# Kernel optimization log

Measured on AMD Instinct MI355X. Metric: run time of the kernel, lower is better.

The kernel has to match this reference:

```python
import jax, jax.numpy as jnp
import numpy as np

B, N, E = 2, 30000, 120000
IN_F, OUT_F, H = 512, 512, 4
D = OUT_F // H  # head_dim = 128
LN_EPS = 1e-5


def setup_inputs() -> dict:
    key = jax.random.key(0)
    k1, k2, k3, k4 = jax.random.split(key, 4)
    node_features = jax.random.normal(k1, (B, N, IN_F), dtype=jnp.float32)
    edge_index = jax.random.randint(k2, (2, E), 0, N, dtype=jnp.int64)
    # per-head linear transforms (bias=False): W[h] is [in_features, head_dim]
    W = jax.random.normal(k3, (H, IN_F, D), dtype=jnp.float32) / np.sqrt(IN_F)
    # per-head attention vectors a[h] is [2*head_dim] (Linear(2*head_dim,1,bias=False))
    a = jax.random.normal(k4, (H, 2 * D), dtype=jnp.float32) / np.sqrt(2 * D)
    ln_gamma = jnp.ones((OUT_F,), dtype=jnp.float32)
    ln_beta = jnp.zeros((OUT_F,), dtype=jnp.float32)
    return {"node_features": node_features, "edge_index": edge_index,
            "W": W, "a": a, "ln_gamma": ln_gamma, "ln_beta": ln_beta}


def reference(node_features, edge_index, W, a, ln_gamma, ln_beta):
    src, dst = edge_index[0], edge_index[1]
    # all-heads linear transform: [B, H, N, D]
    t = jnp.einsum('bni,hid->bhnd', node_features, W)
    # per-edge gathered features: [B, H, E, D]
    sf = t[:, :, src, :]
    df = t[:, :, dst, :]
    # attention score = [sf ; df] . a  == sf.a_src + df.a_dst  -> [B, H, E]
    scores = (jnp.einsum('bhed,hd->bhe', sf, a[:, :D])
              + jnp.einsum('bhed,hd->bhe', df, a[:, D:]))
    scores = jax.nn.leaky_relu(scores, negative_slope=0.2)
    # NOTE: faithful to source — softmax over ALL edges (dim=-1), not per-dst
    w = jax.nn.softmax(scores, axis=-1)
    # scatter-add aggregation into destination nodes (the Python-loop in torch)
    agg = jnp.zeros_like(t).at[:, :, dst, :].add(w[..., None] * sf)  # [B,H,N,D]
    # concat heads along feature dim (head order preserved)
    out = jnp.transpose(agg, (0, 2, 1, 3)).reshape(node_features.shape[0], N, H * D)
    # LayerNorm over last dim
    mu = jnp.mean(out, axis=-1, keepdims=True)
    var = jnp.mean(jnp.square(out - mu), axis=-1, keepdims=True)
    out = (out - mu) * jax.lax.rsqrt(var + LN_EPS) * ln_gamma + ln_beta
    return out
```

## Files before the change

### kernel.cpp

```cpp
#include <hip/hip_runtime.h>
#include <stdint.h>

#define Bn 2
#define Nn 30000
#define En 120000
#define KIN 512
#define Hh 4
#define Dd 128
#define MROWS 60000
#define MPAD  60032
#define LNEPS 1e-5f
#define EBLK 469

typedef unsigned short u16;
typedef unsigned int   u32;
typedef __attribute__((ext_vector_type(8))) short short8;
typedef __attribute__((ext_vector_type(4))) float f32x4;

__device__ __forceinline__ u16 f2bf(float f) {
    u32 u = __builtin_bit_cast(u32, f);
    u32 r = u + 0x7FFFu + ((u >> 16) & 1u);
    return (u16)(r >> 16);
}
__device__ __forceinline__ float bflo(u32 u) {
    return __builtin_bit_cast(float, u << 16);
}
__device__ __forceinline__ float bfhi(u32 u) {
    return __builtin_bit_cast(float, u & 0xFFFF0000u);
}
__device__ __forceinline__ void ld16(void* lds, const void* g) {
    __builtin_amdgcn_global_load_lds((const __attribute__((address_space(1))) void*)g,
                                     (__attribute__((address_space(3))) void*)lds, 16, 0, 0);
}

#define CVTX_BLKS 15008
#define CVTW_BLKS 1024
__global__ void prep_kernel(const float* __restrict__ x, u16* __restrict__ xb,
                            const float* __restrict__ W, u16* __restrict__ wbt,
                            const int* __restrict__ ei, int* __restrict__ deg) {
    int blk = blockIdx.x;
    if (blk < CVTX_BLKS) {
        long base = ((long)blk * 256 + threadIdx.x) * 8;
        short8 o = {};
        if (base < (long)MROWS * KIN) {
            const float4* px = (const float4*)(x + base);
            float4 v0 = px[0], v1 = px[1];
            o[0] = (short)f2bf(v0.x); o[1] = (short)f2bf(v0.y);
            o[2] = (short)f2bf(v0.z); o[3] = (short)f2bf(v0.w);
            o[4] = (short)f2bf(v1.x); o[5] = (short)f2bf(v1.y);
            o[6] = (short)f2bf(v1.z); o[7] = (short)f2bf(v1.w);
        }
        *(short8*)(xb + base) = o;
    } else if (blk < CVTX_BLKS + CVTW_BLKS) {
        int idx = (blk - CVTX_BLKS) * 256 + threadIdx.x;
        int c = idx >> 9, i = idx & 511;
        int h = c >> 7, d = c & 127;
        wbt[idx] = f2bf(W[h * (KIN * Dd) + i * Dd + d]);
    } else {
        int e = (blk - CVTX_BLKS - CVTW_BLKS) * 256 + threadIdx.x;
        if (e < En) atomicAdd(&deg[ei[En + e]], 1);
    }
}

__device__ void scan512(const int* __restrict__ deg, int* __restrict__ offs,
                        int* __restrict__ cursor, int* __restrict__ part) {
    int tid = threadIdx.x;
    const int CH = 59;
    int start = tid * CH;
    int s = 0;
    for (int i = 0; i < CH; i++) {
        int n = start + i;
        if (n < Nn) s += deg[n];
    }
    part[tid] = s;
    __syncthreads();
    for (int off = 1; off < 512; off <<= 1) {
        int xv = (tid >= off) ? part[tid - off] : 0;
        __syncthreads();
        part[tid] += xv;
        __syncthreads();
    }
    int run = part[tid] - s;
    for (int i = 0; i < CH; i++) {
        int n = start + i;
        if (n < Nn) {
            offs[n] = run;
            cursor[n] = run;
            run += deg[n];
        }
    }
    if (tid == 511) offs[Nn] = part[511];
}

#define A_LDS (2 * 128 * 32)
#define B_LDS (2 * 512 * 32)
__launch_bounds__(512)
__global__ void gemm(const u16* __restrict__ xb, const u16* __restrict__ wbt,
                     const float* __restrict__ ag, u16* __restrict__ t,
                     float* __restrict__ s1g, float* __restrict__ s2g,
                     const int* __restrict__ deg, int* __restrict__ offs,
                     int* __restrict__ cursor) {
    __shared__ __align__(16) u16 smem[A_LDS + B_LDS];
    if (blockIdx.x == 0) { scan512(deg, offs, cursor, (int*)smem); return; }
    u16* As0 = smem;
    u16* As1 = smem + 128 * 32;
    u16* Bs0 = smem + A_LDS;
    u16* Bs1 = smem + A_LDS + 512 * 32;
    const int tid = threadIdx.x;
    const int m0 = (blockIdx.x - 1) * 128;
    const int w = tid >> 6, l = tid & 63;
    const int lr = l & 15, lk = l >> 4;
    const int wrM = (w >> 2) * 64;
    const int h = w & 3;
    const int wc = h * 128;
    const int swz = (lk * 8) ^ ((lr & 6) << 2);
    int aoff[4], boff[8];
    #pragma unroll
    for (int mi = 0; mi < 4; mi++) aoff[mi] = (wrM + mi * 16 + lr) * 32 + swz;
    #pragma unroll
    for (int nj = 0; nj < 8; nj++) boff[nj] = (wc + nj * 16 + lr) * 32 + swz;

    const int grow = tid >> 2, gslot = tid & 3;
    const int gsw = (gslot * 8) ^ ((grow & 6) << 2);
    const u16* agsrc = xb + (long)(m0 + grow) * KIN + gsw;
    const u16* bgsrc = wbt + (long)grow * KIN + gsw;
    f32x4 acc[4][8] = {};

    auto STAGE = [&](u16* Ab, u16* Bb, int k0) {
        ld16(Ab + (long)tid * 8, agsrc + k0);
        #pragma unroll
        for (int i = 0; i < 4; i++)
            ld16(Bb + ((long)(i * 512 + tid)) * 8, bgsrc + (long)i * 128 * KIN + k0);
    };

    STAGE(As0, Bs0, 0);
    __syncthreads();
    #pragma unroll 2
    for (int t16 = 0; t16 < 16; t16++) {
        u16* Ac = (t16 & 1) ? As1 : As0;
        u16* Bc = (t16 & 1) ? Bs1 : Bs0;
        if (t16 < 15)
            STAGE((t16 & 1) ? As0 : As1, (t16 & 1) ? Bs0 : Bs1, (t16 + 1) * 32);
        short8 af[4];
        #pragma unroll
        for (int mi = 0; mi < 4; mi++) af[mi] = *(const short8*)&Ac[aoff[mi]];
        #pragma unroll
        for (int nj = 0; nj < 8; nj++) {
            short8 bv = *(const short8*)&Bc[boff[nj]];
            #pragma unroll
            for (int mi = 0; mi < 4; mi++)
                acc[mi][nj] = __builtin_amdgcn_mfma_f32_16x16x32_bf16(
                    af[mi], bv, acc[mi][nj], 0, 0, 0);
        }
        __syncthreads();
    }
    #pragma unroll
    for (int mi = 0; mi < 4; mi++)
        #pragma unroll
        for (int r = 0; r < 4; r++) {
            int row = m0 + wrM + mi * 16 + lk * 4 + r;
            u16* tp = t + (long)row * 512 + wc + lr;
            #pragma unroll
            for (int nj = 0; nj < 8; nj++)
                tp[nj * 16] = f2bf(acc[mi][nj][r]);
        }
    float a1c[8], a2c[8];
    #pragma unroll
    for (int nj = 0; nj < 8; nj++) {
        int col = nj * 16 + lr;
        a1c[nj] = ag[h * 256 + col];
        a2c[nj] = ag[h * 256 + 128 + col];
    }
    float p1[16], p2[16];
    #pragma unroll
    for (int mi = 0; mi < 4; mi++)
        #pragma unroll
        for (int r = 0; r < 4; r++) {
            float v1 = 0.f, v2 = 0.f;
            #pragma unroll
            for (int nj = 0; nj < 8; nj++) {
                float tv = acc[mi][nj][r];
                v1 += tv * a1c[nj];
                v2 += tv * a2c[nj];
            }
            p1[mi * 4 + r] = v1;
            p2[mi * 4 + r] = v2;
        }
    #pragma unroll
    for (int off = 1; off < 16; off <<= 1)
        #pragma unroll
        for (int i = 0; i < 16; i++) {
            p1[i] += __shfl_xor(p1[i], off, 64);
            p2[i] += __shfl_xor(p2[i], off, 64);
        }
    if (lr == 0) {
        #pragma unroll
        for (int mi = 0; mi < 4; mi++)
            #pragma unroll
            for (int r = 0; r < 4; r++) {
                int row = m0 + wrM + mi * 16 + lk * 4 + r;
                if (row < MROWS) {
                    s1g[(long)row * 4 + h] = p1[mi * 4 + r];
                    s2g[(long)row * 4 + h] = p2[mi * 4 + r];
                }
            }
    }
}

__global__ void edgescatter_kernel(const int* __restrict__ ei, const float* __restrict__ s1,
                                   const float* __restrict__ s2, int* __restrict__ cursor,
                                   int* __restrict__ srcs, float* __restrict__ pw,
                                   float* __restrict__ Zpart) {
    int e = blockIdx.x * 256 + threadIdx.x;
    int tid = threadIdx.x;
    float v[8] = {0.f, 0.f, 0.f, 0.f, 0.f, 0.f, 0.f, 0.f};
    if (e < En) {
        int src = ei[e], dst = ei[En + e];
        #pragma unroll
        for (int b = 0; b < Bn; b++) {
            float4 v1 = *(const float4*)(s1 + ((long)b * Nn + src) * 4);
            float4 v2 = *(const float4*)(s2 + ((long)b * Nn + dst) * 4);
            float s;
            s = v1.x + v2.x; s = s > 0.f ? s : 0.2f * s; v[b * 4 + 0] = __expf(s);
            s = v1.y + v2.y; s = s > 0.f ? s : 0.2f * s; v[b * 4 + 1] = __expf(s);
            s = v1.z + v2.z; s = s > 0.f ? s : 0.2f * s; v[b * 4 + 2] = __expf(s);
            s = v1.w + v2.w; s = s > 0.f ? s : 0.2f * s; v[b * 4 + 3] = __expf(s);
        }
        int pos = atomicAdd(&cursor[dst], 1);
        srcs[pos] = src;
        *(float4*)(pw + (long)pos * 4)        = make_float4(v[0], v[1], v[2], v[3]);
        *(float4*)(pw + ((long)En + pos) * 4) = make_float4(v[4], v[5], v[6], v[7]);
    }
    #pragma unroll
    for (int off = 1; off < 64; off <<= 1)
        #pragma unroll
        for (int i = 0; i < 8; i++)
            v[i] += __shfl_xor(v[i], off, 64);
    __shared__ float red[4][8];
    if ((tid & 63) == 0)
        #pragma unroll
        for (int i = 0; i < 8; i++)
            red[tid >> 6][i] = v[i];
    __syncthreads();
    if (tid < 8)
        Zpart[(long)blockIdx.x * 8 + tid] =
            red[0][tid] + red[1][tid] + red[2][tid] + red[3][tid];
}

__global__ void zreduce_kernel(const float* __restrict__ Zpart, float* __restrict__ invZ) {
    int tid = threadIdx.x;
    int g = tid >> 5, l = tid & 31;
    float s = 0.f;
    for (int i = l; i < EBLK; i += 32)
        s += Zpart[(long)i * 8 + g];
    #pragma unroll
    for (int off = 1; off < 32; off <<= 1)
        s += __shfl_xor(s, off, 64);
    if (l == 0) invZ[g] = 1.0f / s;
}

__launch_bounds__(128)
__global__ void agg_kernel(const u16* __restrict__ t, const int* __restrict__ srcs,
                           const float* __restrict__ pw, const float* __restrict__ invZ,
                           const int* __restrict__ offs,
                           const float* __restrict__ gamma, const float* __restrict__ beta,
                           float* __restrict__ out) {
    int tid = threadIdx.x;
    int n = blockIdx.x;
    int b = blockIdx.y;
    int h = tid >> 5;
    int j0 = offs[n], j1 = offs[n + 1];
    const float* pwb = pw + (long)b * En * 4;
    const u16* tb = t + (long)b * Nn * 512;
    float a0 = 0.f, a1 = 0.f, a2 = 0.f, a3 = 0.f;
    int j = j0;
    for (; j + 4 <= j1; j += 4) {
        int s0 = srcs[j], s1i = srcs[j + 1], s2i = srcs[j + 2], s3i = srcs[j + 3];
        float w0 = pwb[(long)j * 4 + h];
        float w1 = pwb[(long)(j + 1) * 4 + h];
        float w2 = pwb[(long)(j + 2) * 4 + h];
        float w3 = pwb[(long)(j + 3) * 4 + h];
        uint2 r0 = *(const uint2*)(tb + (long)s0 * 512 + tid * 4);
        uint2 r1 = *(const uint2*)(tb + (long)s1i * 512 + tid * 4);
        uint2 r2 = *(const uint2*)(tb + (long)s2i * 512 + tid * 4);
        uint2 r3 = *(const uint2*)(tb + (long)s3i * 512 + tid * 4);
        a0 += w0 * bflo(r0.x) + w1 * bflo(r1.x) + w2 * bflo(r2.x) + w3 * bflo(r3.x);
        a1 += w0 * bfhi(r0.x) + w1 * bfhi(r1.x) + w2 * bfhi(r2.x) + w3 * bfhi(r3.x);
        a2 += w0 * bflo(r0.y) + w1 * bflo(r1.y) + w2 * bflo(r2.y) + w3 * bflo(r3.y);
        a3 += w0 * bfhi(r0.y) + w1 * bfhi(r1.y) + w2 * bfhi(r2.y) + w3 * bfhi(r3.y);
    }
    for (; j < j1; j++) {
        int s0 = srcs[j];
        float w0 = pwb[(long)j * 4 + h];
        uint2 r0 = *(const uint2*)(tb + (long)s0 * 512 + tid * 4);
        a0 += w0 * bflo(r0.x);
        a1 += w0 * bfhi(r0.x);
        a2 += w0 * bflo(r0.y);
        a3 += w0 * bfhi(r0.y);
    }
    float invz = invZ[b * 4 + h];
    a0 *= invz; a1 *= invz; a2 *= invz; a3 *= invz;
    float s  = a0 + a1 + a2 + a3;
    float ss = a0 * a0 + a1 * a1 + a2 * a2 + a3 * a3;
    #pragma unroll
    for (int off = 1; off < 64; off <<= 1) {
        s  += __shfl_xor(s, off, 64);
        ss += __shfl_xor(ss, off, 64);
    }
    __shared__ float red[2][2];
    int wv = tid >> 6;
    if ((tid & 63) == 0) { red[wv][0] = s; red[wv][1] = ss; }
    __syncthreads();
    s  = red[0][0] + red[1][0];
    ss = red[0][1] + red[1][1];
    float mean = s * (1.0f / 512.0f);
    float var = ss * (1.0f / 512.0f) - mean * mean;
    var = var < 0.f ? 0.f : var;
    float scale = rsqrtf(var + LNEPS);
    int c = tid * 4;
    float4 o;
    o.x = (a0 - mean) * scale * gamma[c + 0] + beta[c + 0];
    o.y = (a1 - mean) * scale * gamma[c + 1] + beta[c + 1];
    o.z = (a2 - mean) * scale * gamma[c + 2] + beta[c + 2];
    o.w = (a3 - mean) * scale * gamma[c + 3] + beta[c + 3];
    *(float4*)(out + ((long)b * Nn + n) * 512 + c) = o;
}

extern "C" void kernel_launch(void* const* d_in, const int* in_sizes, int n_in,
                              void* d_out, int out_size, void* d_ws, size_t ws_size,
                              hipStream_t stream) {
    const float* x     = (const float*)d_in[0];
    const int*   ei    = (const int*)d_in[1];
    const float* W     = (const float*)d_in[2];
    const float* a     = (const float*)d_in[3];
    const float* gamma = (const float*)d_in[4];
    const float* beta  = (const float*)d_in[5];
    float* out = (float*)d_out;

    char* ws = (char*)d_ws;
    size_t off = 0;
    auto alloc = [&](size_t bytes) -> void* {
        void* ptr = ws + off;
        off = (off + bytes + 255) & ~(size_t)255;
        return ptr;
    };
    u16*   xb     = (u16*)alloc((size_t)MPAD * KIN * 2);
    u16*   wbt    = (u16*)alloc((size_t)512 * 512 * 2);
    u16*   t      = (u16*)alloc((size_t)MPAD * 512 * 2);
    float* s1     = (float*)alloc((size_t)MROWS * 4 * 4);
    float* s2     = (float*)alloc((size_t)MROWS * 4 * 4);
    float* pw     = (float*)alloc((size_t)Bn * En * 4 * 4);
    float* Zpart  = (float*)alloc((size_t)EBLK * 8 * 4);
    float* invZ   = (float*)alloc(8 * 4);
    int*   deg    = (int*)alloc((size_t)Nn * 4);
    int*   offs   = (int*)alloc((size_t)(Nn + 1) * 4);
    int*   cursor = (int*)alloc((size_t)Nn * 4);
    int*   srcs   = (int*)alloc((size_t)En * 4);

    hipMemsetAsync(deg, 0, (size_t)Nn * 4, stream);

    prep_kernel<<<CVTX_BLKS + CVTW_BLKS + EBLK, 256, 0, stream>>>(x, xb, W, wbt, ei, deg);
    gemm<<<470, 512, 0, stream>>>(xb, wbt, a, t, s1, s2, deg, offs, cursor);
    edgescatter_kernel<<<EBLK, 256, 0, stream>>>(ei, s1, s2, cursor, srcs, pw, Zpart);
    zreduce_kernel<<<1, 256, 0, stream>>>(Zpart, invZ);
    agg_kernel<<<dim3(Nn, Bn), 128, 0, stream>>>(t, srcs, pw, invZ, offs, gamma, beta, out);
}
```

Measured before the change: 398.1 us.

## Fuse fp32-to-bf16 conversion of node features into GEMM A-tile loading

The separate pass that converts node features to a bf16 buffer is removed. The GEMM now loads fp32 rows directly into registers two k-steps ahead, converts them, and writes the swizzled bf16 tile to LDS after the MFMA work, while the weight tile still uses direct global-to-LDS loads. This drops a full write and re-read of a roughly 60 MB intermediate, at the cost of more registers and conversion ALU work inside the GEMM. Separately, the aggregation kernel now handles both batches of a node in one 256-thread block, which halves the grid and shares the node's offset lookups.

```diff
diff --git a/kernel.cpp b/kernel.cpp
--- a/kernel.cpp
+++ b/kernel.cpp
@@ -33,31 +33,17 @@
                                      (__attribute__((address_space(3))) void*)lds, 16, 0, 0);
 }
 
-#define CVTX_BLKS 15008
 #define CVTW_BLKS 1024
-__global__ void prep_kernel(const float* __restrict__ x, u16* __restrict__ xb,
-                            const float* __restrict__ W, u16* __restrict__ wbt,
+__global__ void prep_kernel(const float* __restrict__ W, u16* __restrict__ wbt,
                             const int* __restrict__ ei, int* __restrict__ deg) {
     int blk = blockIdx.x;
-    if (blk < CVTX_BLKS) {
-        long base = ((long)blk * 256 + threadIdx.x) * 8;
-        short8 o = {};
-        if (base < (long)MROWS * KIN) {
-            const float4* px = (const float4*)(x + base);
-            float4 v0 = px[0], v1 = px[1];
-            o[0] = (short)f2bf(v0.x); o[1] = (short)f2bf(v0.y);
-            o[2] = (short)f2bf(v0.z); o[3] = (short)f2bf(v0.w);
-            o[4] = (short)f2bf(v1.x); o[5] = (short)f2bf(v1.y);
-            o[6] = (short)f2bf(v1.z); o[7] = (short)f2bf(v1.w);
-        }
-        *(short8*)(xb + base) = o;
-    } else if (blk < CVTX_BLKS + CVTW_BLKS) {
-        int idx = (blk - CVTX_BLKS) * 256 + threadIdx.x;
+    if (blk < CVTW_BLKS) {
+        int idx = blk * 256 + threadIdx.x;
         int c = idx >> 9, i = idx & 511;
         int h = c >> 7, d = c & 127;
         wbt[idx] = f2bf(W[h * (KIN * Dd) + i * Dd + d]);
     } else {
-        int e = (blk - CVTX_BLKS - CVTW_BLKS) * 256 + threadIdx.x;
+        int e = (blk - CVTW_BLKS) * 256 + threadIdx.x;
         if (e < En) atomicAdd(&deg[ei[En + e]], 1);
     }
 }
@@ -95,7 +81,7 @@
 #define A_LDS (2 * 128 * 32)
 #define B_LDS (2 * 512 * 32)
 __launch_bounds__(512)
-__global__ void gemm(const u16* __restrict__ xb, const u16* __restrict__ wbt,
+__global__ void gemm(const float* __restrict__ x, const u16* __restrict__ wbt,
                      const float* __restrict__ ag, u16* __restrict__ t,
                      float* __restrict__ s1g, float* __restrict__ s2g,
                      const int* __restrict__ deg, int* __restrict__ offs,
@@ -120,40 +106,75 @@
     #pragma unroll
     for (int nj = 0; nj < 8; nj++) boff[nj] = (wc + nj * 16 + lr) * 32 + swz;
 
+    const int arow_u = m0 + (tid >> 2);
+    const int arow = arow_u < MROWS ? arow_u : (MROWS - 1);
+    const float* xsrc = x + (long)arow * KIN + (tid & 3) * 8;
+    const int awr = (tid >> 2) * 32 + (((tid & 3) * 8) ^ (((tid >> 2) & 6) << 2));
+
     const int grow = tid >> 2, gslot = tid & 3;
     const int gsw = (gslot * 8) ^ ((grow & 6) << 2);
-    const u16* agsrc = xb + (long)(m0 + grow) * KIN + gsw;
     const u16* bgsrc = wbt + (long)grow * KIN + gsw;
     f32x4 acc[4][8] = {};
-
-    auto STAGE = [&](u16* Ab, u16* Bb, int k0) {
-        ld16(Ab + (long)tid * 8, agsrc + k0);
+    float4 a0A, a1A, a0B, a1B;
+
+#define LOADX(R0, R1, KS)                                           \
+    {                                                               \
+        R0 = *(const float4*)(xsrc + (KS) * 32);                    \
+        R1 = *(const float4*)(xsrc + (KS) * 32 + 4);                \
+    }
+#define CVTW(BUF, R0, R1)                                           \
+    {                                                               \
+        short8 o;                                                   \
+        o[0] = (short)f2bf(R0.x); o[1] = (short)f2bf(R0.y);         \
+        o[2] = (short)f2bf(R0.z); o[3] = (short)f2bf(R0.w);         \
+        o[4] = (short)f2bf(R1.x); o[5] = (short)f2bf(R1.y);         \
+        o[6] = (short)f2bf(R1.z); o[7] = (short)f2bf(R1.w);         \
+        *(short8*)&(BUF)[awr] = o;                                  \
+    }
+
+    auto STAGEB = [&](u16* Bb, int k0) {
         #pragma unroll
         for (int i = 0; i < 4; i++)
             ld16(Bb + ((long)(i * 512 + tid)) * 8, bgsrc + (long)i * 128 * KIN + k0);
     };
 
-    STAGE(As0, Bs0, 0);
+    LOADX(a0A, a1A, 0);
+    LOADX(a0B, a1B, 1);
+    STAGEB(Bs0, 0);
+    CVTW(As0, a0A, a1A);
     __syncthreads();
-    #pragma unroll 2
+
+    #pragma unroll
     for (int t16 = 0; t16 < 16; t16++) {
-        u16* Ac = (t16 & 1) ? As1 : As0;
-        u16* Bc = (t16 & 1) ? Bs1 : Bs0;
-        if (t16 < 15)
-            STAGE((t16 & 1) ? As0 : As1, (t16 & 1) ? Bs0 : Bs1, (t16 + 1) * 32);
+        u16* Acur = (t16 & 1) ? As1 : As0;
+        u16* Bcur = (t16 & 1) ? Bs1 : Bs0;
+        u16* Anext = (t16 & 1) ? As0 : As1;
+        u16* Bnext = (t16 & 1) ? Bs0 : Bs1;
+        if (t16 < 14) {
+            if (t16 & 1) { LOADX(a0B, a1B, t16 + 2); }
+            else         { LOADX(a0A, a1A, t16 + 2); }
+        }
+        if (t16 < 15) STAGEB(Bnext, (t16 + 1) * 32);
         short8 af[4];
         #pragma unroll
-        for (int mi = 0; mi < 4; mi++) af[mi] = *(const short8*)&Ac[aoff[mi]];
+        for (int mi = 0; mi < 4; mi++) af[mi] = *(const short8*)&Acur[aoff[mi]];
         #pragma unroll
         for (int nj = 0; nj < 8; nj++) {
-            short8 bv = *(const short8*)&Bc[boff[nj]];
+            short8 bv = *(const short8*)&Bcur[boff[nj]];
             #pragma unroll
             for (int mi = 0; mi < 4; mi++)
                 acc[mi][nj] = __builtin_amdgcn_mfma_f32_16x16x32_bf16(
                     af[mi], bv, acc[mi][nj], 0, 0, 0);
         }
+        if (t16 < 15) {
+            if (t16 & 1) { CVTW(Anext, a0A, a1A); }
+            else         { CVTW(Anext, a0B, a1B); }
+        }
         __syncthreads();
     }
+#undef LOADX
+#undef CVTW
+
     #pragma unroll
     for (int mi = 0; mi < 4; mi++)
         #pragma unroll
@@ -259,16 +280,17 @@
     if (l == 0) invZ[g] = 1.0f / s;
 }
 
-__launch_bounds__(128)
+__launch_bounds__(256)
 __global__ void agg_kernel(const u16* __restrict__ t, const int* __restrict__ srcs,
                            const float* __restrict__ pw, const float* __restrict__ invZ,
                            const int* __restrict__ offs,
                            const float* __restrict__ gamma, const float* __restrict__ beta,
                            float* __restrict__ out) {
     int tid = threadIdx.x;
+    int b = tid >> 7;
+    int lt = tid & 127;
     int n = blockIdx.x;
-    int b = blockIdx.y;
-    int h = tid >> 5;
+    int h = lt >> 5;
     int j0 = offs[n], j1 = offs[n + 1];
     const float* pwb = pw + (long)b * En * 4;
     const u16* tb = t + (long)b * Nn * 512;
@@ -280,10 +302,10 @@
         float w1 = pwb[(long)(j + 1) * 4 + h];
         float w2 = pwb[(long)(j + 2) * 4 + h];
         float w3 = pwb[(long)(j + 3) * 4 + h];
-        uint2 r0 = *(const uint2*)(tb + (long)s0 * 512 + tid * 4);
-        uint2 r1 = *(const uint2*)(tb + (long)s1i * 512 + tid * 4);
-        uint2 r2 = *(const uint2*)(tb + (long)s2i * 512 + tid * 4);
-        uint2 r3 = *(const uint2*)(tb + (long)s3i * 512 + tid * 4);
+        uint2 r0 = *(const uint2*)(tb + (long)s0 * 512 + lt * 4);
+        uint2 r1 = *(const uint2*)(tb + (long)s1i * 512 + lt * 4);
+        uint2 r2 = *(const uint2*)(tb + (long)s2i * 512 + lt * 4);
+        uint2 r3 = *(const uint2*)(tb + (long)s3i * 512 + lt * 4);
         a0 += w0 * bflo(r0.x) + w1 * bflo(r1.x) + w2 * bflo(r2.x) + w3 * bflo(r3.x);
         a1 += w0 * bfhi(r0.x) + w1 * bfhi(r1.x) + w2 * bfhi(r2.x) + w3 * bfhi(r3.x);
         a2 += w0 * bflo(r0.y) + w1 * bflo(r1.y) + w2 * bflo(r2.y) + w3 * bflo(r3.y);
@@ -292,7 +314,7 @@
     for (; j < j1; j++) {
         int s0 = srcs[j];
         float w0 = pwb[(long)j * 4 + h];
-        uint2 r0 = *(const uint2*)(tb + (long)s0 * 512 + tid * 4);
+        uint2 r0 = *(const uint2*)(tb + (long)s0 * 512 + lt * 4);
         a0 += w0 * bflo(r0.x);
         a1 += w0 * bfhi(r0.x);
         a2 += w0 * bflo(r0.y);
@@ -307,17 +329,17 @@
         s  += __shfl_xor(s, off, 64);
         ss += __shfl_xor(ss, off, 64);
     }
-    __shared__ float red[2][2];
+    __shared__ float red[4][2];
     int wv = tid >> 6;
     if ((tid & 63) == 0) { red[wv][0] = s; red[wv][1] = ss; }
     __syncthreads();
-    s  = red[0][0] + red[1][0];
-    ss = red[0][1] + red[1][1];
+    s  = red[b * 2][0] + red[b * 2 + 1][0];
+    ss = red[b * 2][1] + red[b * 2 + 1][1];
     float mean = s * (1.0f / 512.0f);
     float var = ss * (1.0f / 512.0f) - mean * mean;
     var = var < 0.f ? 0.f : var;
     float scale = rsqrtf(var + LNEPS);
-    int c = tid * 4;
+    int c = lt * 4;
     float4 o;
     o.x = (a0 - mean) * scale * gamma[c + 0] + beta[c + 0];
     o.y = (a1 - mean) * scale * gamma[c + 1] + beta[c + 1];
@@ -344,7 +366,6 @@
         off = (off + bytes + 255) & ~(size_t)255;
         return ptr;
     };
-    u16*   xb     = (u16*)alloc((size_t)MPAD * KIN * 2);
     u16*   wbt    = (u16*)alloc((size_t)512 * 512 * 2);
     u16*   t      = (u16*)alloc((size_t)MPAD * 512 * 2);
     float* s1     = (float*)alloc((size_t)MROWS * 4 * 4);
@@ -359,9 +380,9 @@
 
     hipMemsetAsync(deg, 0, (size_t)Nn * 4, stream);
 
-    prep_kernel<<<CVTX_BLKS + CVTW_BLKS + EBLK, 256, 0, stream>>>(x, xb, W, wbt, ei, deg);
-    gemm<<<470, 512, 0, stream>>>(xb, wbt, a, t, s1, s2, deg, offs, cursor);
+    prep_kernel<<<CVTW_BLKS + EBLK, 256, 0, stream>>>(W, wbt, ei, deg);
+    gemm<<<470, 512, 0, stream>>>(x, wbt, a, t, s1, s2, deg, offs, cursor);
     edgescatter_kernel<<<EBLK, 256, 0, stream>>>(ei, s1, s2, cursor, srcs, pw, Zpart);
     zreduce_kernel<<<1, 256, 0, stream>>>(Zpart, invZ);
-    agg_kernel<<<dim3(Nn, Bn), 128, 0, stream>>>(t, srcs, pw, invZ, offs, gamma, beta, out);
-}
+    agg_kernel<<<Nn, 256, 0, stream>>>(t, srcs, pw, invZ, offs, gamma, beta, out);
+}
```

New measurement: 361.2 us. 9.3% less time.
